# Kernel tuning notes

Hardware: AMD Instinct MI355X
Metric: run time of the kernel (lower is better)

The kernel has to match this reference:

```python
import jax, jax.numpy as jnp
import numpy as np

NUM_STATES = 4096
SEQ_LEN = 4096


def setup_inputs() -> dict:
    key = jax.random.key(0)
    k1, k2, k3, k4 = jax.random.split(key, 4)
    state_dist = jax.random.uniform(k1, (NUM_STATES,), dtype=jnp.float32)
    input_seq = jax.random.randint(k2, (SEQ_LEN,), 0, 2, dtype=jnp.int64)
    T = jax.random.normal(k3, (NUM_STATES, 2, NUM_STATES), dtype=jnp.float32) * 0.1
    O = jax.random.normal(k4, (NUM_STATES, 2, 4), dtype=jnp.float32) * 0.1
    return {"state_dist": state_dist, "input_seq": input_seq, "T": T, "O": O}


def reference(state_dist, input_seq, T, O):
    # Softmax over last dim -> row-stochastic transition / emission matrices.
    Tm = jax.nn.softmax(T, axis=-1)  # [N, 2, N]
    Om = jax.nn.softmax(O, axis=-1)  # [N, 2, 4]

    def step(state, sym):
        # (O[:, sym, :] * state[:, None]).sum(0) == state @ O[:, sym, :]
        O_s = jnp.take(Om, sym, axis=1)          # [N, 4]
        T_s = jnp.take(Tm, sym, axis=1)          # [N, N]
        out_prob = state @ O_s                    # [4]
        new_state = state @ T_s                   # [N]
        return new_state, out_prob

    _, outputs = jax.lax.scan(step, state_dist, input_seq)
    return outputs  # [L, 4]
```

## Files before the change

kernel.cpp:

```cpp
#include <hip/hip_runtime.h>
#include <hip/hip_fp16.h>

#define N 4096
#define L 4096
#define NPART 16
#define NJB 32
#define CPB 128
#define RPB 256

#define NN ((size_t)N * (size_t)N)
#define SLOT ((size_t)N * 4)
#define VTN ((size_t)NPART * N)

#define ASU(p, v) __hip_atomic_store((p), (v), __ATOMIC_RELAXED, __HIP_MEMORY_SCOPE_AGENT)
#define ALU(p)    __hip_atomic_load((p), __ATOMIC_RELAXED, __HIP_MEMORY_SCOPE_AGENT)

typedef _Float16 f16x8 __attribute__((ext_vector_type(8)));
typedef float f32x4 __attribute__((ext_vector_type(4)));

__global__ __launch_bounds__(256) void init_kernel(const float* __restrict__ sd,
                                                   unsigned long long* __restrict__ vt,
                                                   float* __restrict__ rcacc,
                                                   float* __restrict__ out) {
    int g = blockIdx.x * 256 + threadIdx.x;
    if (g < L * 4) out[g] = 0.0f;
    if (g < (int)(3 * VTN)) {
        float val = (g < N) ? sd[g] : 0.0f;
        ASU(&vt[g], (unsigned long long)__float_as_uint(val));
    }
    if (g < 16 * N) rcacc[g] = 0.0f;
}

__global__ __launch_bounds__(256) void build_desc_kernel(const int* __restrict__ seq32,
                                                         unsigned char* __restrict__ midx,
                                                         int mode) {
    __shared__ int any_odd;
    if (threadIdx.x == 0) any_odd = 0;
    __syncthreads();
    int acc = 0;
    for (int i = threadIdx.x; i < L / 2; i += 256) acc |= seq32[2 * i + 1];
    if (acc) any_odd = 1;
    __syncthreads();
    const int is64 = (any_odd == 0);
#define SYM(t) ((is64 ? seq32[2 * (t)] : seq32[(t)]) & 1)
    if (mode == 2) {
        for (int k = threadIdx.x; k < L / 4; k += 256)
            midx[k] = (unsigned char)(SYM(4 * k) * 8 + SYM(4 * k + 1) * 4 +
                                      SYM(4 * k + 2) * 2 + SYM(4 * k + 3));
    } else if (mode == 1) {
        for (int k = threadIdx.x; k < L / 2; k += 256)
            midx[k] = (unsigned char)(SYM(2 * k) * 2 + SYM(2 * k + 1));
    } else {
        for (int t = threadIdx.x; t < L; t += 256)
            midx[t] = (unsigned char)SYM(t);
    }
#undef SYM
}

__global__ __launch_bounds__(256) void softmax_T_kernel(const float* __restrict__ T,
                                                        unsigned short* __restrict__ Tm,
                                                        float* __restrict__ rowc) {
    int row = blockIdx.x;
    int i = row >> 1, s = row & 1;
    const float* src = T + (size_t)row * N;
    unsigned short* dst = Tm + ((size_t)s << 24) + ((size_t)i << 12);
    int tid = threadIdx.x;

    float vals[16];
    float mx = -1e30f;
#pragma unroll
    for (int k = 0; k < 16; k++) {
        vals[k] = src[tid + (k << 8)];
        mx = fmaxf(mx, vals[k]);
    }
#pragma unroll
    for (int o = 32; o > 0; o >>= 1) mx = fmaxf(mx, __shfl_xor(mx, o));
    __shared__ float red[4];
    int wid = tid >> 6;
    if ((tid & 63) == 0) red[wid] = mx;
    __syncthreads();
    mx = fmaxf(fmaxf(red[0], red[1]), fmaxf(red[2], red[3]));
    __syncthreads();

    float sum = 0.0f;
#pragma unroll
    for (int k = 0; k < 16; k++) {
        vals[k] = __expf(vals[k] - mx);
        sum += vals[k];
    }
#pragma unroll
    for (int o = 32; o > 0; o >>= 1) sum += __shfl_xor(sum, o);
    if ((tid & 63) == 0) red[wid] = sum;
    __syncthreads();
    sum = red[0] + red[1] + red[2] + red[3];
    __syncthreads();
    float inv = 1.0f / sum;

    float qs = 0.0f;
#pragma unroll
    for (int k = 0; k < 16; k++) {
        __half h = __float2half_rn(vals[k] * inv);
        dst[tid + (k << 8)] = __half_as_ushort(h);
        qs += __half2float(h);
    }
#pragma unroll
    for (int o = 32; o > 0; o >>= 1) qs += __shfl_xor(qs, o);
    if ((tid & 63) == 0) red[wid] = qs;
    __syncthreads();
    if (tid == 0) {
        float q = red[0] + red[1] + red[2] + red[3];
        rowc[(size_t)s * N + i] = 1.0f / q;
    }
}

__global__ __launch_bounds__(256) void softmax_O_kernel(const float* __restrict__ O,
                                                        float* __restrict__ OW) {
    int r = blockIdx.x * 256 + threadIdx.x;
    if (r < 2 * N) {
        float4 x = *(const float4*)(O + (size_t)r * 4);
        float mx = fmaxf(fmaxf(x.x, x.y), fmaxf(x.z, x.w));
        float e0 = __expf(x.x - mx), e1 = __expf(x.y - mx);
        float e2 = __expf(x.z - mx), e3 = __expf(x.w - mx);
        float inv = 1.0f / (e0 + e1 + e2 + e3);
        int i = r >> 1, s = r & 1;
        *(float4*)(OW + (size_t)s * SLOT + (size_t)i * 4) =
            make_float4(e0 * inv, e1 * inv, e2 * inv, e3 * inv);
    }
}

template <int Q8OUT>
__global__ __launch_bounds__(256) void gemm_kernel(const unsigned short* __restrict__ Abase,
                                                   const unsigned short* __restrict__ Bbase,
                                                   void* __restrict__ Cbase,
                                                   float* __restrict__ rcacc,
                                                   int ash, int bmask) {
    const int nwg = gridDim.x;
    int bid0 = blockIdx.x;
    int bid = (bid0 & 7) * (nwg >> 3) + (bid0 >> 3);
    int pair = bid >> 10;
    int tile = bid & 1023;
    int i0 = (tile >> 5) << 7;
    int j0 = (tile & 31) << 7;
    const unsigned short* A = Abase + (size_t)(pair >> ash) * NN;
    const unsigned short* B = Bbase + (size_t)(pair & bmask) * NN;

    __shared__ _Float16 Asd[128 * 64];
    __shared__ unsigned int Btw[128][36];

    const int tid = threadIdx.x;
    const int w = tid >> 6, ln = tid & 63;
    const int wrow = (w >> 1) << 6, wcol = (w & 1) << 6;
    const int q = ln >> 4, l15 = ln & 15;

    const int kp = tid & 31, cgB = tid >> 5;

    const int gA = (ln & 7) ^ (ln >> 3);

    f32x4 acc[4][4] = {};

    for (int k0 = 0; k0 < N; k0 += 64) {
#pragma unroll
        for (int t = 0; t < 4; t++) {
            const int rbase = w * 32 + t * 8;
            const int r = rbase + (ln >> 3);
            __builtin_amdgcn_global_load_lds(
                (const __attribute__((address_space(1))) unsigned int*)
                    (A + (size_t)(i0 + r) * N + k0 + gA * 8),
                (__attribute__((address_space(3))) unsigned int*)(Asd + rbase * 64),
                16, 0, 0);
        }
        const unsigned short* gb0 = B + (size_t)(k0 + 2 * kp) * N + j0 + cgB * 16;
        uint4 b0  = *(const uint4*)gb0;
        uint4 b0h = *(const uint4*)(gb0 + 8);
        uint4 b1  = *(const uint4*)(gb0 + N);
        uint4 b1h = *(const uint4*)(gb0 + N + 8);
        const unsigned short* e0  = (const unsigned short*)&b0;
        const unsigned short* e1  = (const unsigned short*)&b1;
        const unsigned short* e0h = (const unsigned short*)&b0h;
        const unsigned short* e1h = (const unsigned short*)&b1h;
#pragma unroll
        for (int jj = 0; jj < 8; jj++)
            Btw[cgB * 16 + jj][kp] = (unsigned)e0[jj] | ((unsigned)e1[jj] << 16);
#pragma unroll
        for (int jj = 0; jj < 8; jj++)
            Btw[cgB * 16 + 8 + jj][kp] = (unsigned)e0h[jj] | ((unsigned)e1h[jj] << 16);
        __syncthreads();

#pragma unroll
        for (int kk = 0; kk < 2; kk++) {
            f16x8 af[4], bf[4];
#pragma unroll
            for (int ti = 0; ti < 4; ti++) {
                const int R = wrow + ti * 16 + l15;
                const int G = (kk * 4 + q) ^ (l15 & 7);
                af[ti] = *(const f16x8*)(Asd + R * 64 + G * 8);
            }
#pragma unroll
            for (int tj = 0; tj < 4; tj++)
                bf[tj] = *(const f16x8*)&Btw[wcol + tj * 16 + l15][kk * 16 + q * 4];
#pragma unroll
            for (int ti = 0; ti < 4; ti++)
#pragma unroll
                for (int tj = 0; tj < 4; tj++)
                    acc[ti][tj] = __builtin_amdgcn_mfma_f32_16x16x32_f16(
                        af[ti], bf[tj], acc[ti][tj], 0, 0, 0);
        }
        __syncthreads();
    }

    if (Q8OUT == 0) {
        unsigned short* Pm = (unsigned short*)Cbase + (size_t)pair * NN;
#pragma unroll
        for (int ti = 0; ti < 4; ti++)
#pragma unroll
            for (int tj = 0; tj < 4; tj++)
#pragma unroll
                for (int reg = 0; reg < 4; reg++) {
                    int row = i0 + wrow + ti * 16 + q * 4 + reg;
                    int col = j0 + wcol + tj * 16 + l15;
                    Pm[(size_t)row * N + col] =
                        __half_as_ushort(__float2half_rn(acc[ti][tj][reg]));
                }
    } else {
        unsigned char* Pm8 = (unsigned char*)Cbase + (size_t)pair * NN;
        float* rcrow = rcacc + (size_t)pair * N;
#pragma unroll
        for (int ti = 0; ti < 4; ti++)
#pragma unroll
            for (int reg = 0; reg < 4; reg++) {
                int row = i0 + wrow + ti * 16 + q * 4 + reg;
                float rs = 0.0f;
#pragma unroll
                for (int tj = 0; tj < 4; tj++) {
                    float f = acc[ti][tj][reg] * 16384.0f;
                    unsigned hb = __half_as_ushort(__float2half_rn(f));
                    unsigned r = hb + 0x3Fu + ((hb >> 7) & 1u);
                    int qv = (int)(r >> 7) - 64;
                    qv = qv < 8 ? 8 : (qv > 0x7E ? 0x7E : qv);
                    unsigned short db = (unsigned short)((qv + 64) << 7);
                    rs += __half2float(*reinterpret_cast<const __half*>(&db));
                    Pm8[(size_t)row * N + j0 + wcol + tj * 16 + l15] = (unsigned char)qv;
                }
                rs += __shfl_xor(rs, 1); rs += __shfl_xor(rs, 2);
                rs += __shfl_xor(rs, 4); rs += __shfl_xor(rs, 8);
                if (l15 == 0) atomicAdd(&rcrow[row], rs);
            }
    }
}

__global__ __launch_bounds__(256) void rcinv_kernel(float* __restrict__ rc) {
    int g = blockIdx.x * 256 + threadIdx.x;
    if (g < 16 * N) rc[g] = 1.0f / rc[g];
}

__global__ __launch_bounds__(256) void rowsum_kernel(const unsigned short* __restrict__ P,
                                                     float* __restrict__ rc) {
    int b = blockIdx.x;
    const unsigned short* row = P + (size_t)b * N;
    int tid = threadIdx.x;
    const uint4* rp = (const uint4*)row + tid * 2;
    uint4 w0 = rp[0], w1 = rp[1];
    const __half* h0 = (const __half*)&w0;
    const __half* h1 = (const __half*)&w1;
    float s = 0.0f;
#pragma unroll
    for (int j = 0; j < 8; j++) s += __half2float(h0[j]) + __half2float(h1[j]);
#pragma unroll
    for (int o = 32; o > 0; o >>= 1) s += __shfl_xor(s, o);
    __shared__ float red[4];
    if ((tid & 63) == 0) red[tid >> 6] = s;
    __syncthreads();
    if (tid == 0) rc[b] = 1.0f / (red[0] + red[1] + red[2] + red[3]);
}

__global__ __launch_bounds__(256) void proj_kernel(const unsigned short* __restrict__ Tm,
                                                   const unsigned short* __restrict__ P,
                                                   const float* __restrict__ rowc,
                                                   const float* __restrict__ rowc2,
                                                   float* __restrict__ OW, int phase) {
    int bid = blockIdx.x;
    int s = bid >> 12, i = bid & 4095;
    const unsigned short* M; const float* rc; const float* Q; float* dst;
    if (phase == 1) {
        if (s < 4) { M = Tm + (size_t)(s >> 1) * NN; rc = rowc + (size_t)(s >> 1) * N;
                     Q = OW + (size_t)(s & 1) * SLOT; dst = OW + (size_t)(2 + s) * SLOT; }
        else { int q = s - 4; M = P + (size_t)(q >> 1) * NN; rc = rowc2 + (size_t)(q >> 1) * N;
               Q = OW + (size_t)(q & 1) * SLOT; dst = OW + (size_t)(6 + q) * SLOT; }
    } else {
        int q = s; M = P + (size_t)(q >> 2) * NN; rc = rowc2 + (size_t)(q >> 2) * N;
        Q = OW + (size_t)(2 + (q & 3)) * SLOT; dst = OW + (size_t)(14 + q) * SLOT;
    }
    const unsigned short* row = M + (size_t)i * N;
    int tid = threadIdx.x;
    const uint4* rp = (const uint4*)row + tid * 2;
    uint4 w0 = rp[0], w1 = rp[1];
    const __half* h0 = (const __half*)&w0;
    const __half* h1 = (const __half*)&w1;
    int j0 = tid * 16;
    float ac[4] = {};
#pragma unroll
    for (int j = 0; j < 8; j++) {
        float tv = __half2float(h0[j]);
        float4 o = *(const float4*)(Q + (size_t)(j0 + j) * 4);
        ac[0] += tv * o.x; ac[1] += tv * o.y; ac[2] += tv * o.z; ac[3] += tv * o.w;
        float tv1 = __half2float(h1[j]);
        float4 o1 = *(const float4*)(Q + (size_t)(j0 + 8 + j) * 4);
        ac[0] += tv1 * o1.x; ac[1] += tv1 * o1.y; ac[2] += tv1 * o1.z; ac[3] += tv1 * o1.w;
    }
#pragma unroll
    for (int e = 0; e < 4; e++)
#pragma unroll
        for (int o = 32; o > 0; o >>= 1) ac[e] += __shfl_xor(ac[e], o);
    __shared__ float red[4][4];
    if ((tid & 63) == 0)
#pragma unroll
        for (int e = 0; e < 4; e++) red[tid >> 6][e] = ac[e];
    __syncthreads();
    if (tid < 4)
        dst[(size_t)i * 4 + tid] =
            (red[0][tid] + red[1][tid] + red[2][tid] + red[3][tid]) * rc[i];
}

__device__ __forceinline__ float2 d8x2(unsigned b0, unsigned b1) {
    unsigned pk = ((b0 + 64u) << 7) | ((b1 + 64u) << 23);
    return __half22float2(*reinterpret_cast<__half2*>(&pk));
}

#define SPIN_SUM(vinp, kk, accv)                                               \
    {                                                                          \
        unsigned long long uv[16];                                             \
        _Pragma("unroll")                                                      \
        for (int p = 0; p < 16; p++) uv[p] = ALU((vinp) + p * N);              \
        unsigned miss = 0;                                                     \
        _Pragma("unroll")                                                      \
        for (int p = 0; p < 16; p++)                                           \
            if ((unsigned)(uv[p] >> 32) != (kk)) miss |= 1u << p;              \
        while (__builtin_expect(miss != 0, 0)) {                               \
            _Pragma("unroll")                                                  \
            for (int p = 0; p < 16; p++)                                       \
                if (miss & (1u << p)) {                                        \
                    unsigned long long t = ALU((vinp) + p * N);                \
                    if ((unsigned)(t >> 32) == (kk)) { uv[p] = t; miss &= ~(1u << p); } \
                }                                                              \
        }                                                                      \
        _Pragma("unroll")                                                      \
        for (int p = 0; p < 16; p++) accv += __uint_as_float((unsigned)uv[p]); \
    }

__global__ __launch_bounds__(256, 2) void scan8_kernel(const unsigned char* __restrict__ Q8,
                                                       const float* __restrict__ rc,
                                                       const float* __restrict__ OW,
                                                       const unsigned char* __restrict__ midx,
                                                       unsigned long long* __restrict__ vt,
                                                       float* __restrict__ out,
                                                       int S, int OPS) {
    const int tid = threadIdx.x;
    const int jb = blockIdx.x & 31;
    const int ic = blockIdx.x >> 5;
    const int i0 = ic * RPB;
    const int j0 = jb * CPB;

    __shared__ unsigned char mt8[2][RPB][CPB];
    __shared__ float v[RPB];
    __shared__ float vc[RPB];
    __shared__ float colacc[CPB];

    const int cg = tid & 15;
    const int rg = tid >> 4;

    const int w4 = tid >> 6;
    const int ln = tid & 63;
    const size_t goff8 = (size_t)(i0 + (ln >> 3)) * N + j0 + (ln & 7) * 16;

#define STAGE8(Mb, dst)                                                         \
    _Pragma("unroll")                                                           \
    for (int t = 0; t < 8; t++) {                                               \
        const int row0 = w4 * 64 + t * 8;                                       \
        __builtin_amdgcn_global_load_lds(                                       \
            (const __attribute__((address_space(1))) unsigned int*)((Mb) + goff8 + (size_t)row0 * N), \
            (__attribute__((address_space(3))) unsigned int*)((dst) + (size_t)row0 * CPB),            \
            16, 0, 0);                                                          \
    }

    int mcur = (int)midx[0];
    int mnxt = (S > 1) ? (int)midx[1] : 0;
    float rc_cur = rc[(size_t)mcur * N + i0 + tid];
    float rc_nxt = (S > 1) ? rc[(size_t)mnxt * N + i0 + tid] : 0.0f;
    STAGE8(Q8 + (size_t)mcur * NN, &mt8[0][0][0]);

    for (int k = 0; k < S; k++) {
        const int m = mcur;
        const unsigned long long* vinp = vt + (size_t)(k % 3) * VTN + (i0 + tid);
        unsigned long long* voutp = vt + (size_t)((k + 1) % 3) * VTN + (size_t)ic * N + j0;
        const unsigned char* mtc = &mt8[k & 1][0][0];

        float accv = 0.0f;
        SPIN_SUM(vinp, (unsigned)k, accv);
        v[tid] = accv;
        vc[tid] = accv * rc_cur;
        if (tid < CPB) colacc[tid] = 0.0f;

        if (k + 1 < S) {
            STAGE8(Q8 + (size_t)mnxt * NN, &mt8[(k + 1) & 1][0][0]);
            asm volatile("s_waitcnt vmcnt(8) lgkmcnt(0)" ::: "memory");
        } else {
            asm volatile("s_waitcnt vmcnt(0) lgkmcnt(0)" ::: "memory");
        }
        __builtin_amdgcn_s_barrier();
        __builtin_amdgcn_sched_barrier(0);

        float a[8];
#pragma unroll
        for (int e = 0; e < 8; e++) a[e] = 0.0f;
#pragma unroll
        for (int r = 0; r < 16; r++) {
            uint2 w = *(const uint2*)(mtc + (size_t)(rg * 16 + r) * CPB + cg * 8);
            float vi = vc[rg * 16 + r];
            float2 f0 = d8x2(w.x & 0xFF, (w.x >> 8) & 0xFF);
            float2 f1 = d8x2((w.x >> 16) & 0xFF, w.x >> 24);
            float2 f2 = d8x2(w.y & 0xFF, (w.y >> 8) & 0xFF);
            float2 f3 = d8x2((w.y >> 16) & 0xFF, w.y >> 24);
            a[0] += vi * f0.x; a[1] += vi * f0.y;
            a[2] += vi * f1.x; a[3] += vi * f1.y;
            a[4] += vi * f2.x; a[5] += vi * f2.y;
            a[6] += vi * f3.x; a[7] += vi * f3.y;
        }
#pragma unroll
        for (int e = 0; e < 8; e++) atomicAdd(&colacc[cg * 8 + e], a[e]);

        if (jb < OPS) {
            int slot;
            if (OPS == 4) slot = (jb == 0) ? (m >> 3) : (jb == 1) ? 2 + (m >> 2)
                               : (jb == 2) ? 6 + (m >> 1) : 14 + m;
            else if (OPS == 2) slot = (jb == 0) ? (m >> 1) : 2 + m;
            else slot = m;
            const float* pr = OW + (size_t)slot * SLOT;
            int r = tid >> 2, c = tid & 3;
            float p = v[r]       * pr[(size_t)(i0 + r) * 4 + c]
                    + v[r + 64]  * pr[(size_t)(i0 + r + 64) * 4 + c]
                    + v[r + 128] * pr[(size_t)(i0 + r + 128) * 4 + c]
                    + v[r + 192] * pr[(size_t)(i0 + r + 192) * 4 + c];
            p += __shfl_down(p, 32); p += __shfl_down(p, 16);
            p += __shfl_down(p, 8);  p += __shfl_down(p, 4);
            if ((tid & 63) < 4) atomicAdd(&out[(k * OPS + jb) * 4 + (tid & 3)], p);
        }

        asm volatile("s_waitcnt lgkmcnt(0)" ::: "memory");
        __builtin_amdgcn_s_barrier();
        __builtin_amdgcn_sched_barrier(0);

        if (tid < CPB) {
            unsigned long long pk = ((unsigned long long)(unsigned)(k + 1) << 32)
                                  | (unsigned long long)__float_as_uint(colacc[tid]);
            ASU(&voutp[tid], pk);
        }
        mcur = mnxt; rc_cur = rc_nxt;
        if (k + 2 < S) {
            mnxt = (int)midx[k + 2];
            rc_nxt = rc[(size_t)mnxt * N + i0 + tid];
        }
    }
#undef STAGE8
}

__global__ __launch_bounds__(256, 2) void scan16_kernel(const unsigned short* __restrict__ Mbase,
                                                        const float* __restrict__ rc,
                                                        const float* __restrict__ OW,
                                                        const unsigned char* __restrict__ midx,
                                                        unsigned long long* __restrict__ vt,
                                                        float* __restrict__ out,
                                                        int S, int OPS) {
    const int tid = threadIdx.x;
    const int jb = blockIdx.x & 31;
    const int ic = blockIdx.x >> 5;
    const int i0 = ic * RPB;
    const int j0 = jb * CPB;

    __shared__ unsigned short mt[RPB][CPB];
    __shared__ float v[RPB];
    __shared__ float vc[RPB];
    __shared__ float colacc[CPB];

    const int cg = tid & 15;
    const int rg = tid >> 4;

    const int w4 = tid >> 6;
    const int ln = tid & 63;
    const size_t goff = (size_t)(i0 + (ln >> 4)) * N + j0 + (ln & 15) * 8;

    int mcur = (int)midx[0];
    int mnxt = (S > 1) ? (int)midx[1] : 0;
    float rc_cur = rc[(size_t)mcur * N + i0 + tid];
    float rc_nxt = (S > 1) ? rc[(size_t)mnxt * N + i0 + tid] : 0.0f;
    {
        const unsigned short* Mb = Mbase + (size_t)mcur * NN;
#pragma unroll
        for (int t = 0; t < 16; t++) {
            const int row0 = w4 * 64 + t * 4;
            __builtin_amdgcn_global_load_lds(
                (const __attribute__((address_space(1))) unsigned int*)(Mb + goff + (size_t)row0 * N),
                (__attribute__((address_space(3))) unsigned int*)(&mt[row0][0]),
                16, 0, 0);
        }
    }

    for (int k = 0; k < S; k++) {
        const int m = mcur;
        const unsigned long long* vinp = vt + (size_t)(k % 3) * VTN + (i0 + tid);
        unsigned long long* voutp = vt + (size_t)((k + 1) % 3) * VTN + (size_t)ic * N + j0;

        float accv = 0.0f;
        SPIN_SUM(vinp, (unsigned)k, accv);
        v[tid] = accv;
        vc[tid] = accv * rc_cur;
        if (tid < CPB) colacc[tid] = 0.0f;
        __syncthreads();

        float a[8];
#pragma unroll
        for (int e = 0; e < 8; e++) a[e] = 0.0f;
#pragma unroll
        for (int r = 0; r < 16; r++) {
            uint4 w = *(const uint4*)&mt[rg * 16 + r][cg * 8];
            float vi = vc[rg * 16 + r];
            float2 f0 = __half22float2(*(__half2*)&w.x);
            float2 f1 = __half22float2(*(__half2*)&w.y);
            float2 f2 = __half22float2(*(__half2*)&w.z);
            float2 f3 = __half22float2(*(__half2*)&w.w);
            a[0] += vi * f0.x; a[1] += vi * f0.y;
            a[2] += vi * f1.x; a[3] += vi * f1.y;
            a[4] += vi * f2.x; a[5] += vi * f2.y;
            a[6] += vi * f3.x; a[7] += vi * f3.y;
        }
#pragma unroll
        for (int e = 0; e < 8; e++) atomicAdd(&colacc[cg * 8 + e], a[e]);

        if (jb < OPS) {
            int slot;
            if (OPS == 4) slot = (jb == 0) ? (m >> 3) : (jb == 1) ? 2 + (m >> 2)
                               : (jb == 2) ? 6 + (m >> 1) : 14 + m;
            else if (OPS == 2) slot = (jb == 0) ? (m >> 1) : 2 + m;
            else slot = m;
            const float* pr = OW + (size_t)slot * SLOT;
            int r = tid >> 2, c = tid & 3;
            float p = v[r]       * pr[(size_t)(i0 + r) * 4 + c]
                    + v[r + 64]  * pr[(size_t)(i0 + r + 64) * 4 + c]
                    + v[r + 128] * pr[(size_t)(i0 + r + 128) * 4 + c]
                    + v[r + 192] * pr[(size_t)(i0 + r + 192) * 4 + c];
            p += __shfl_down(p, 32); p += __shfl_down(p, 16);
            p += __shfl_down(p, 8);  p += __shfl_down(p, 4);
            if ((tid & 63) < 4) atomicAdd(&out[(k * OPS + jb) * 4 + (tid & 3)], p);
        }
        __syncthreads();

        if (tid < CPB) {
            unsigned long long pk = ((unsigned long long)(unsigned)(k + 1) << 32)
                                  | (unsigned long long)__float_as_uint(colacc[tid]);
            ASU(&voutp[tid], pk);
        }
        if (k + 1 < S) {
            const unsigned short* Mb = Mbase + (size_t)mnxt * NN;
#pragma unroll
            for (int t = 0; t < 16; t++) {
                const int row0 = w4 * 64 + t * 4;
                __builtin_amdgcn_global_load_lds(
                    (const __attribute__((address_space(1))) unsigned int*)(Mb + goff + (size_t)row0 * N),
                    (__attribute__((address_space(3))) unsigned int*)(&mt[row0][0]),
                    16, 0, 0);
            }
        }
        mcur = mnxt; rc_cur = rc_nxt;
        if (k + 2 < S) {
            mnxt = (int)midx[k + 2];
            rc_nxt = rc[(size_t)mnxt * N + i0 + tid];
        }
    }
}

extern "C" void kernel_launch(void* const* d_in, const int* in_sizes, int n_in,
                              void* d_out, int out_size, void* d_ws, size_t ws_size,
                              hipStream_t stream) {
    const float* sd  = (const float*)d_in[0];
    const int*   seq = (const int*)d_in[1];
    const float* T   = (const float*)d_in[2];
    const float* O   = (const float*)d_in[3];
    float* out = (float*)d_out;

    const size_t TM_SZ = 2 * NN * 2;
    const size_t P_SZ  = 4 * NN * 2;
    const size_t Q8_SZ = 16 * NN;
    const size_t AUX_SZ = 0x400000;

    int mode = (ws_size >= TM_SZ + P_SZ + Q8_SZ + AUX_SZ) ? 3
             : (ws_size >= TM_SZ + P_SZ + AUX_SZ) ? 1 : 0;

    char* ws = (char*)d_ws;
    unsigned short* Tm = (unsigned short*)ws;
    unsigned short* P  = (unsigned short*)(ws + TM_SZ);
    unsigned char*  Q8 = (unsigned char*)(ws + TM_SZ + P_SZ);
    char* aux = ws + (mode == 3 ? TM_SZ + P_SZ + Q8_SZ
                    : mode == 1 ? TM_SZ + P_SZ : TM_SZ);
    float* rowc   = (float*)(aux);
    float* rowc2  = (float*)(aux + 0x8000);
    float* rowc4  = (float*)(aux + 0x18000);
    float* OW     = (float*)(aux + 0x58000);
    unsigned long long* vt = (unsigned long long*)(aux + 0x258000);
    unsigned char* midx = (unsigned char*)(aux + 0x3D8000);

    hipLaunchKernelGGL(init_kernel, dim3(1536), dim3(256), 0, stream, sd, vt, rowc4, out);
    hipLaunchKernelGGL(build_desc_kernel, dim3(1), dim3(256), 0, stream, seq, midx,
                       mode == 3 ? 2 : mode);
    hipLaunchKernelGGL(softmax_T_kernel, dim3(2 * N), dim3(256), 0, stream, T, Tm, rowc);
    hipLaunchKernelGGL(softmax_O_kernel, dim3(32), dim3(256), 0, stream, O, OW);

    if (mode == 3) {
        hipLaunchKernelGGL(HIP_KERNEL_NAME(gemm_kernel<0>), dim3(4 * 1024), dim3(256), 0, stream,
                           Tm, Tm, (void*)P, rowc4, 1, 1);
        hipLaunchKernelGGL(rowsum_kernel, dim3(4 * N), dim3(256), 0, stream, P, rowc2);
        hipLaunchKernelGGL(HIP_KERNEL_NAME(gemm_kernel<1>), dim3(16 * 1024), dim3(256), 0, stream,
                           P, P, (void*)Q8, rowc4, 2, 3);
        hipLaunchKernelGGL(rcinv_kernel, dim3(256), dim3(256), 0, stream, rowc4);
        hipLaunchKernelGGL(proj_kernel, dim3(12 * N), dim3(256), 0, stream, Tm, P, rowc, rowc2, OW, 1);
        hipLaunchKernelGGL(proj_kernel, dim3(16 * N), dim3(256), 0, stream, Tm, P, rowc, rowc2, OW, 2);
        hipLaunchKernelGGL(scan8_kernel, dim3(512), dim3(256), 0, stream,
                           Q8, rowc4, OW, midx, vt, out, L / 4, 4);
    } else if (mode == 1) {
        hipLaunchKernelGGL(HIP_KERNEL_NAME(gemm_kernel<0>), dim3(4 * 1024), dim3(256), 0, stream,
                           Tm, Tm, (void*)P, rowc4, 1, 1);
        hipLaunchKernelGGL(rowsum_kernel, dim3(4 * N), dim3(256), 0, stream, P, rowc2);
        hipLaunchKernelGGL(proj_kernel, dim3(4 * N), dim3(256), 0, stream, Tm, P, rowc, rowc2, OW, 1);
        hipLaunchKernelGGL(scan16_kernel, dim3(512), dim3(256), 0, stream,
                           P, rowc2, OW, midx, vt, out, L / 2, 2);
    } else {
        hipLaunchKernelGGL(scan16_kernel, dim3(512), dim3(256), 0, stream,
                           Tm, rowc, OW, midx, vt, out, L, 1);
    }
}
```

Measured before the change: 15.36 ms.

## Pre-transpose GEMM B operands so both tiles load via async global-to-LDS

Adds a transpose kernel that writes transposed copies of the softmaxed transition matrices and the P products into extra workspace. The GEMM then loads B tiles with the same global_load_lds swizzled path as A, replacing the register-staged interleave into a padded LDS array. This removes per-iteration VGPR shuffling and scalar LDS stores in the GEMM main loop. The cost is extra transpose passes over 2 and 4 matrices of 4096x4096, plus a larger workspace requirement, which could push execution into a lower mode if the workspace is too small.

```diff
diff --git a/kernel.cpp b/kernel.cpp
--- a/kernel.cpp
+++ b/kernel.cpp
@@ -128,9 +128,34 @@
     }
 }
 
+__global__ __launch_bounds__(256) void transpose_kernel(const unsigned short* __restrict__ src,
+                                                        unsigned short* __restrict__ dst) {
+    int b = blockIdx.x;
+    int mat = b >> 12;
+    int t = b & 4095;
+    int ti = t >> 6, tj = t & 63;
+    const unsigned short* S = src + (size_t)mat * NN + (size_t)(ti * 64) * N + tj * 64;
+    unsigned short* D = dst + (size_t)mat * NN + (size_t)(tj * 64) * N + ti * 64;
+
+    __shared__ unsigned short tile[64][72];
+
+    int tid = threadIdx.x;
+    int r = tid >> 2, c0 = (tid & 3) * 16;
+    *(uint4*)&tile[r][c0]     = *(const uint4*)(S + (size_t)r * N + c0);
+    *(uint4*)&tile[r][c0 + 8] = *(const uint4*)(S + (size_t)r * N + c0 + 8);
+    __syncthreads();
+
+    int j = tid >> 2, i0 = (tid & 3) * 16;
+    unsigned short g[16];
+#pragma unroll
+    for (int s = 0; s < 16; s++) g[s] = tile[i0 + s][j];
+    *(uint4*)(D + (size_t)j * N + i0)     = *(const uint4*)&g[0];
+    *(uint4*)(D + (size_t)j * N + i0 + 8) = *(const uint4*)&g[8];
+}
+
 template <int Q8OUT>
 __global__ __launch_bounds__(256) void gemm_kernel(const unsigned short* __restrict__ Abase,
-                                                   const unsigned short* __restrict__ Bbase,
+                                                   const unsigned short* __restrict__ BTbase,
                                                    void* __restrict__ Cbase,
                                                    float* __restrict__ rcacc,
                                                    int ash, int bmask) {
@@ -141,18 +166,16 @@
     int tile = bid & 1023;
     int i0 = (tile >> 5) << 7;
     int j0 = (tile & 31) << 7;
-    const unsigned short* A = Abase + (size_t)(pair >> ash) * NN;
-    const unsigned short* B = Bbase + (size_t)(pair & bmask) * NN;
+    const unsigned short* A  = Abase  + (size_t)(pair >> ash) * NN;
+    const unsigned short* BT = BTbase + (size_t)(pair & bmask) * NN;
 
     __shared__ _Float16 Asd[128 * 64];
-    __shared__ unsigned int Btw[128][36];
+    __shared__ _Float16 Bsd[128 * 64];
 
     const int tid = threadIdx.x;
     const int w = tid >> 6, ln = tid & 63;
     const int wrow = (w >> 1) << 6, wcol = (w & 1) << 6;
     const int q = ln >> 4, l15 = ln & 15;
-
-    const int kp = tid & 31, cgB = tid >> 5;
 
     const int gA = (ln & 7) ^ (ln >> 3);
 
@@ -169,21 +192,16 @@
                 (__attribute__((address_space(3))) unsigned int*)(Asd + rbase * 64),
                 16, 0, 0);
         }
-        const unsigned short* gb0 = B + (size_t)(k0 + 2 * kp) * N + j0 + cgB * 16;
-        uint4 b0  = *(const uint4*)gb0;
-        uint4 b0h = *(const uint4*)(gb0 + 8);
-        uint4 b1  = *(const uint4*)(gb0 + N);
-        uint4 b1h = *(const uint4*)(gb0 + N + 8);
-        const unsigned short* e0  = (const unsigned short*)&b0;
-        const unsigned short* e1  = (const unsigned short*)&b1;
-        const unsigned short* e0h = (const unsigned short*)&b0h;
-        const unsigned short* e1h = (const unsigned short*)&b1h;
-#pragma unroll
-        for (int jj = 0; jj < 8; jj++)
-            Btw[cgB * 16 + jj][kp] = (unsigned)e0[jj] | ((unsigned)e1[jj] << 16);
-#pragma unroll
-        for (int jj = 0; jj < 8; jj++)
-            Btw[cgB * 16 + 8 + jj][kp] = (unsigned)e0h[jj] | ((unsigned)e1h[jj] << 16);
+#pragma unroll
+        for (int t = 0; t < 4; t++) {
+            const int rbase = w * 32 + t * 8;
+            const int r = rbase + (ln >> 3);
+            __builtin_amdgcn_global_load_lds(
+                (const __attribute__((address_space(1))) unsigned int*)
+                    (BT + (size_t)(j0 + r) * N + k0 + gA * 8),
+                (__attribute__((address_space(3))) unsigned int*)(Bsd + rbase * 64),
+                16, 0, 0);
+        }
         __syncthreads();
 
 #pragma unroll
@@ -196,8 +214,11 @@
                 af[ti] = *(const f16x8*)(Asd + R * 64 + G * 8);
             }
 #pragma unroll
-            for (int tj = 0; tj < 4; tj++)
-                bf[tj] = *(const f16x8*)&Btw[wcol + tj * 16 + l15][kk * 16 + q * 4];
+            for (int tj = 0; tj < 4; tj++) {
+                const int R = wcol + tj * 16 + l15;
+                const int G = (kk * 4 + q) ^ (l15 & 7);
+                bf[tj] = *(const f16x8*)(Bsd + R * 64 + G * 8);
+            }
 #pragma unroll
             for (int ti = 0; ti < 4; ti++)
 #pragma unroll
@@ -591,15 +612,17 @@
     const size_t Q8_SZ = 16 * NN;
     const size_t AUX_SZ = 0x400000;
 
-    int mode = (ws_size >= TM_SZ + P_SZ + Q8_SZ + AUX_SZ) ? 3
-             : (ws_size >= TM_SZ + P_SZ + AUX_SZ) ? 1 : 0;
+    int mode = (ws_size >= 2 * TM_SZ + 2 * P_SZ + Q8_SZ + AUX_SZ) ? 3
+             : (ws_size >= 2 * TM_SZ + P_SZ + AUX_SZ) ? 1 : 0;
 
     char* ws = (char*)d_ws;
-    unsigned short* Tm = (unsigned short*)ws;
-    unsigned short* P  = (unsigned short*)(ws + TM_SZ);
-    unsigned char*  Q8 = (unsigned char*)(ws + TM_SZ + P_SZ);
-    char* aux = ws + (mode == 3 ? TM_SZ + P_SZ + Q8_SZ
-                    : mode == 1 ? TM_SZ + P_SZ : TM_SZ);
+    unsigned short* Tm  = (unsigned short*)ws;
+    unsigned short* TmT = (unsigned short*)(ws + TM_SZ);
+    unsigned short* P   = (unsigned short*)(ws + 2 * TM_SZ);
+    unsigned short* PT  = (unsigned short*)(ws + 2 * TM_SZ + P_SZ);
+    unsigned char*  Q8  = (unsigned char*)(ws + 2 * TM_SZ + 2 * P_SZ);
+    char* aux = ws + (mode == 3 ? 2 * TM_SZ + 2 * P_SZ + Q8_SZ
+                    : mode == 1 ? 2 * TM_SZ + P_SZ : TM_SZ);
     float* rowc   = (float*)(aux);
     float* rowc2  = (float*)(aux + 0x8000);
     float* rowc4  = (float*)(aux + 0x18000);
@@ -614,19 +637,22 @@
     hipLaunchKernelGGL(softmax_O_kernel, dim3(32), dim3(256), 0, stream, O, OW);
 
     if (mode == 3) {
+        hipLaunchKernelGGL(transpose_kernel, dim3(2 * 4096), dim3(256), 0, stream, Tm, TmT);
         hipLaunchKernelGGL(HIP_KERNEL_NAME(gemm_kernel<0>), dim3(4 * 1024), dim3(256), 0, stream,
-                           Tm, Tm, (void*)P, rowc4, 1, 1);
+                           Tm, TmT, (void*)P, rowc4, 1, 1);
         hipLaunchKernelGGL(rowsum_kernel, dim3(4 * N), dim3(256), 0, stream, P, rowc2);
+        hipLaunchKernelGGL(transpose_kernel, dim3(4 * 4096), dim3(256), 0, stream, P, PT);
         hipLaunchKernelGGL(HIP_KERNEL_NAME(gemm_kernel<1>), dim3(16 * 1024), dim3(256), 0, stream,
-                           P, P, (void*)Q8, rowc4, 2, 3);
+                           P, PT, (void*)Q8, rowc4, 2, 3);
         hipLaunchKernelGGL(rcinv_kernel, dim3(256), dim3(256), 0, stream, rowc4);
         hipLaunchKernelGGL(proj_kernel, dim3(12 * N), dim3(256), 0, stream, Tm, P, rowc, rowc2, OW, 1);
         hipLaunchKernelGGL(proj_kernel, dim3(16 * N), dim3(256), 0, stream, Tm, P, rowc, rowc2, OW, 2);
         hipLaunchKernelGGL(scan8_kernel, dim3(512), dim3(256), 0, stream,
                            Q8, rowc4, OW, midx, vt, out, L / 4, 4);
     } else if (mode == 1) {
+        hipLaunchKernelGGL(transpose_kernel, dim3(2 * 4096), dim3(256), 0, stream, Tm, TmT);
         hipLaunchKernelGGL(HIP_KERNEL_NAME(gemm_kernel<0>), dim3(4 * 1024), dim3(256), 0, stream,
-                           Tm, Tm, (void*)P, rowc4, 1, 1);
+                           Tm, TmT, (void*)P, rowc4, 1, 1);
         hipLaunchKernelGGL(rowsum_kernel, dim3(4 * N), dim3(256), 0, stream, P, rowc2);
         hipLaunchKernelGGL(proj_kernel, dim3(4 * N), dim3(256), 0, stream, Tm, P, rowc, rowc2, OW, 1);
         hipLaunchKernelGGL(scan16_kernel, dim3(512), dim3(256), 0, stream,
```

After: 20.13 ms. +31.1%, slower.
